# Kernel optimization log

Hardware: AMD Instinct MI355X
Metric: run time of the kernel (lower is better)

Reference implementation:

```python
import jax, jax.numpy as jnp
import numpy as np

B, S, M_DIM, N_DIM, K_NNZ = 8, 2048, 2048, 2048, 205


def setup_inputs() -> dict:
    key = jax.random.key(0)
    k1, k2, k3, k4 = jax.random.split(key, 4)
    x = jax.random.normal(k1, (B, S, M_DIM), dtype=jnp.float32)
    # CSR structure: K_NNZ unique, sorted column indices per row
    scores = jax.random.uniform(k2, (N_DIM, M_DIM))
    cols = jnp.sort(jnp.argsort(scores, axis=1)[:, :K_NNZ], axis=1)  # [N, K] unique per row
    indices = cols.reshape(-1).astype(jnp.int32)                      # [nnz]
    indptr = (jnp.arange(N_DIM + 1) * K_NNZ).astype(jnp.int32)        # [N+1]
    W_val = jax.random.normal(k3, (N_DIM * K_NNZ,), dtype=jnp.float32) * (1.0 / np.sqrt(M_DIM))
    bias = jax.random.normal(k4, (N_DIM,), dtype=jnp.float32) * 0.01
    return {"x": x, "W_val": W_val, "bias": bias, "indices": indices, "indptr": indptr}


def reference(x, W_val, bias, indices, indptr):
    # SparseLinear.forward: y = x @ W^T + bias, with W stored in CSR
    # (W_val: nnz values, indptr: [N+1] row pointers, indices: [nnz] column ids).
    N = indptr.shape[0] - 1
    M = x.shape[-1]
    nnz = W_val.shape[0]
    # row id of each nonzero, derived from indptr (standard CSR expansion)
    row_ids = jnp.searchsorted(indptr, jnp.arange(nnz, dtype=indptr.dtype), side="right") - 1
    # materialize the sparse weight (CSR columns are unique per row -> set is exact)
    W = jnp.zeros((N, M), dtype=W_val.dtype).at[row_ids, indices].set(W_val)
    return jnp.einsum("bsm,nm->bsn", x, W) + bias
```

## Files before the change

### kernel.cpp

```cpp
#include <hip/hip_runtime.h>
#include <hip/hip_bf16.h>
#include <stdint.h>

#define M_TOT 16384
#define K_TOT 2048
#define N_TOT 2048

#define BM 256
#define BN 256
#define BK 64
#define LDS_HALF (128 * 64)

typedef __attribute__((ext_vector_type(8))) short short8;
typedef __attribute__((ext_vector_type(4))) float float4v;
typedef __attribute__((ext_vector_type(8))) unsigned short ushort8;
typedef __attribute__((ext_vector_type(4))) unsigned short ushort4v;

__device__ __forceinline__ unsigned short f2bf_rne(float f) {
    union { float f; unsigned u; } a; a.f = f;
    unsigned r = a.u + 0x7FFFu + ((a.u >> 16) & 1u);
    return (unsigned short)(r >> 16);
}

__global__ __launch_bounds__(256) void densify_kernel(
    const float* __restrict__ val, const int* __restrict__ idx,
    const int* __restrict__ indptr, unsigned short* __restrict__ Wb) {
    const int n = blockIdx.x;
    unsigned short* row = Wb + (size_t)n * K_TOT;
    ushort8 z = {0, 0, 0, 0, 0, 0, 0, 0};
    ((ushort8*)row)[threadIdx.x] = z;
    __syncthreads();
    const int s = indptr[n], e = indptr[n + 1];
    for (int j = s + (int)threadIdx.x; j < e; j += (int)blockDim.x)
        row[idx[j]] = f2bf_rne(val[j]);
}

#define CAST_GRID 2048
__global__ __launch_bounds__(256) void cast_kernel(
    const float* __restrict__ x, unsigned short* __restrict__ xb) {
    const float4* xf = (const float4*)x;
    size_t i = (size_t)blockIdx.x * 256 + threadIdx.x;
    const size_t stride = (size_t)CAST_GRID * 256;
#pragma unroll
    for (int it = 0; it < 16; ++it, i += stride) {
        float4 a = xf[i];
        ushort4v o;
        o[0] = f2bf_rne(a.x); o[1] = f2bf_rne(a.y);
        o[2] = f2bf_rne(a.z); o[3] = f2bf_rne(a.w);
        ((ushort4v*)xb)[i] = o;
    }
}

__global__ __launch_bounds__(512, 2) void gemm_bias_kernel_256(
    const unsigned short* __restrict__ A,
    const unsigned short* __restrict__ Bw,
    const float* __restrict__ bias,
    float* __restrict__ C)
{
    extern __shared__ unsigned short lds[];

    const int tid  = threadIdx.x;
    const int lane = tid & 63;
    const int wave = tid >> 6;

    const int raw = blockIdx.x;
    const int lid = (raw & 7) * 64 + (raw >> 3);
    const int bm = lid >> 3;
    const int bn = lid & 7;

    const int wrow = wave >> 2;
    const int wcol = wave & 3;
    const int wr16 = wrow * 16;
    const int wc16 = wcol * 16;
    const int mrow = lane & 15;
    const int quad = lane >> 4;
    const int rx   = mrow & 7;

    const int srow = lane >> 3;
    const int csrc = ((lane & 7) ^ srow) * 8;
    const unsigned short* pA = A  + (size_t)(bm * BM + wave * 8 + srow) * K_TOT + csrc;
    const unsigned short* pB = Bw + (size_t)(bn * BN + wave * 8 + srow) * K_TOT + csrc;
    unsigned short* lw = lds + wave * 8 * 64;

    float4v acc[8][4] = {};
    short8 af[4][2];
    short8 bfr[2][2][2];

#define STAGE(PG, MATIDX, BUF, H, K0)                                            \
    { _Pragma("unroll")                                                          \
      for (int l = 0; l < 2; ++l) {                                              \
        const unsigned short* g = (PG) + ((size_t)((H) * 128 + l * 64) * K_TOT + (size_t)(K0)); \
        unsigned short* lp = lw + (((BUF) * 4 + (MATIDX) * 2 + (H)) * LDS_HALF) + l * 64 * 64;  \
        __builtin_amdgcn_global_load_lds(                                        \
            (const __attribute__((address_space(1))) unsigned int*)g,            \
            (__attribute__((address_space(3))) unsigned int*)lp, 16, 0, 0);      \
      } }

#define RD_A(RBUF, RMH)                                                          \
    { const unsigned short* Ah = lds + ((RBUF) * 4 + (RMH)) * LDS_HALF;          \
      _Pragma("unroll")                                                          \
      for (int mi = 0; mi < 4; ++mi) {                                           \
        const int r = mi * 32 + wr16 + mrow;                                     \
        _Pragma("unroll")                                                        \
        for (int ks = 0; ks < 2; ++ks)                                           \
          af[mi][ks] = *(const short8*)(Ah + r * 64 + (((ks * 4 + quad) ^ rx) * 8)); \
      } }

#define RD_B(RBUF, RNH)                                                          \
    { const unsigned short* Bh = lds + ((RBUF) * 4 + 2 + (RNH)) * LDS_HALF;      \
      _Pragma("unroll")                                                          \
      for (int ni = 0; ni < 2; ++ni) {                                           \
        const int r = ni * 64 + wc16 + mrow;                                     \
        _Pragma("unroll")                                                        \
        for (int ks = 0; ks < 2; ++ks)                                           \
          bfr[RNH][ni][ks] = *(const short8*)(Bh + r * 64 + (((ks * 4 + quad) ^ rx) * 8)); \
      } }

#define BARX { asm volatile("" ::: "memory"); __builtin_amdgcn_s_barrier(); asm volatile("" ::: "memory"); }
#define NOB  ((void)0);
#define WAITV4 asm volatile("s_waitcnt vmcnt(4)" ::: "memory")
#define WAITV0 asm volatile("s_waitcnt vmcnt(0)" ::: "memory")
#define WV4B { WAITV4; BARX }
#define WV0B { WAITV0; BARX }
#define NOWT ((void)0)
#define NOSTG ((void)0)
#define NORD ((void)0)

#define PHASE(MH, NH, BHEAD, STG, TAILW, RDS)                                    \
  {                                                                              \
    BHEAD                                                                        \
    asm volatile("s_waitcnt lgkmcnt(0)" ::: "memory");                           \
    __builtin_amdgcn_s_setprio(1);                                               \
    _Pragma("unroll")                                                            \
    for (int mi = 0; mi < 4; ++mi)                                               \
      _Pragma("unroll")                                                          \
      for (int ni = 0; ni < 2; ++ni)                                             \
        _Pragma("unroll")                                                        \
        for (int ks = 0; ks < 2; ++ks)                                           \
          acc[(MH) * 4 + mi][(NH) * 2 + ni] =                                    \
              __builtin_amdgcn_mfma_f32_16x16x32_bf16(                           \
                  af[mi][ks], bfr[NH][ni][ks], acc[(MH) * 4 + mi][(NH) * 2 + ni], 0, 0, 0); \
    __builtin_amdgcn_s_setprio(0);                                               \
    STG;                                                                         \
    TAILW;                                                                       \
    RDS;                                                                         \
  }

    STAGE(pA, 0, 0, 0, 0);
    STAGE(pB, 1, 0, 1, 0);
    STAGE(pB, 1, 0, 0, 0);
    STAGE(pA, 0, 0, 1, 0);
    STAGE(pA, 0, 1, 0, 64);
    STAGE(pB, 1, 1, 1, 64);
    WAITV4;
    BARX
    RD_A(0, 0); RD_B(0, 0);

    int k0b = 64, k0c = 128, k0d = 192;
#pragma unroll 1
    for (int it = 0; it < 15; ++it) {
        PHASE(0, 0, NOB,  STAGE(pB, 1, 1, 0, k0b), NOWT, RD_B(0, 1))
        PHASE(0, 1, BARX, STAGE(pA, 0, 1, 1, k0b), NOWT, RD_A(0, 1))
        PHASE(1, 1, BARX, STAGE(pA, 0, 0, 0, k0c), NOWT, NORD)
        PHASE(1, 0, BARX, STAGE(pB, 1, 0, 1, k0c), WV4B, RD_A(1, 0); RD_B(1, 0))
        PHASE(0, 0, NOB,  STAGE(pB, 1, 0, 0, k0c), NOWT, RD_B(1, 1))
        PHASE(0, 1, BARX, STAGE(pA, 0, 0, 1, k0c), NOWT, RD_A(1, 1))
        PHASE(1, 1, BARX, STAGE(pA, 0, 1, 0, k0d), NOWT, NORD)
        PHASE(1, 0, BARX, STAGE(pB, 1, 1, 1, k0d), WV4B, RD_A(0, 0); RD_B(0, 0))
        k0b += 128; k0c += 128; k0d += 128;
    }
    PHASE(0, 0, NOB,  STAGE(pB, 1, 1, 0, k0b), NOWT, RD_B(0, 1))
    PHASE(0, 1, BARX, STAGE(pA, 0, 1, 1, k0b), NOWT, RD_A(0, 1))
    PHASE(1, 1, BARX, NOSTG, NOWT, NORD)
    PHASE(1, 0, BARX, NOSTG, WV0B, RD_A(1, 0); RD_B(1, 0))
    PHASE(0, 0, NOB,  NOSTG, NOWT, RD_B(1, 1))
    PHASE(0, 1, BARX, NOSTG, NOWT, RD_A(1, 1))
    PHASE(1, 1, BARX, NOSTG, NOWT, NORD)
    PHASE(1, 0, BARX, NOSTG, NOWT, NORD)

#pragma unroll
    for (int nh = 0; nh < 2; ++nh)
#pragma unroll
        for (int ni = 0; ni < 2; ++ni) {
            const int col = bn * BN + nh * 128 + ni * 64 + wc16 + mrow;
            const float bv = bias[col];
#pragma unroll
            for (int mh = 0; mh < 2; ++mh)
#pragma unroll
                for (int mi = 0; mi < 4; ++mi) {
                    const int row0 = bm * BM + mh * 128 + mi * 32 + wr16 + quad * 4;
#pragma unroll
                    for (int r = 0; r < 4; ++r)
                        C[(size_t)(row0 + r) * N_TOT + col] =
                            acc[mh * 4 + mi][nh * 2 + ni][r] + bv;
                }
        }
#undef PHASE
#undef STAGE
#undef RD_A
#undef RD_B
#undef BARX
#undef NOB
#undef WAITV4
#undef WAITV0
#undef WV4B
#undef WV0B
#undef NOWT
#undef NOSTG
#undef NORD
}

#define FBM 128
#define FBN 128
#define FBK 64
__global__ __launch_bounds__(256) void gemm_bias_kernel_128(
    const unsigned short* __restrict__ A,
    const unsigned short* __restrict__ Bw,
    const float* __restrict__ bias,
    float* __restrict__ C)
{
    __shared__ unsigned short Asm[FBM * FBK];
    __shared__ unsigned short Bsm[FBN * FBK];

    const int tid  = threadIdx.x;
    const int lane = tid & 63;
    const int wave = tid >> 6;
    const int bm = blockIdx.y;
    const int bn = blockIdx.x;

    const int srow_l = lane >> 3;
    const int schunk = ((lane & 7) ^ srow_l) * 8;
    const unsigned short* a_g[4];
    const unsigned short* b_g[4];
    unsigned short* a_l[4];
    unsigned short* b_l[4];
#pragma unroll
    for (int l = 0; l < 4; ++l) {
        const int row = wave * 32 + l * 8 + srow_l;
        a_g[l] = A  + (size_t)(bm * FBM + row) * K_TOT + schunk;
        b_g[l] = Bw + (size_t)(bn * FBN + row) * K_TOT + schunk;
        a_l[l] = Asm + (wave * 32 + l * 8) * FBK;
        b_l[l] = Bsm + (wave * 32 + l * 8) * FBK;
    }

    const int wm = (wave >> 1) * 64;
    const int wn = (wave & 1) * 64;
    const int mrow = lane & 15;
    const int quad = lane >> 4;
    const int rx   = mrow & 7;

    float4v acc[4][4] = {};

    for (int k0 = 0; k0 < K_TOT; k0 += FBK) {
        __syncthreads();
#pragma unroll
        for (int l = 0; l < 4; ++l)
            __builtin_amdgcn_global_load_lds(
                (const __attribute__((address_space(1))) unsigned int*)(a_g[l] + k0),
                (__attribute__((address_space(3))) unsigned int*)a_l[l], 16, 0, 0);
#pragma unroll
        for (int l = 0; l < 4; ++l)
            __builtin_amdgcn_global_load_lds(
                (const __attribute__((address_space(1))) unsigned int*)(b_g[l] + k0),
                (__attribute__((address_space(3))) unsigned int*)b_l[l], 16, 0, 0);
        __syncthreads();

#pragma unroll
        for (int ks = 0; ks < 2; ++ks) {
            short8 af[4], bf_[4];
#pragma unroll
            for (int mi = 0; mi < 4; ++mi) {
                const int r = wm + mi * 16 + mrow;
                const int slot = (ks * 4 + quad) ^ rx;
                af[mi] = *(const short8*)(Asm + r * FBK + slot * 8);
            }
#pragma unroll
            for (int ni = 0; ni < 4; ++ni) {
                const int r = wn + ni * 16 + mrow;
                const int slot = (ks * 4 + quad) ^ rx;
                bf_[ni] = *(const short8*)(Bsm + r * FBK + slot * 8);
            }
#pragma unroll
            for (int mi = 0; mi < 4; ++mi)
#pragma unroll
                for (int ni = 0; ni < 4; ++ni)
                    acc[mi][ni] = __builtin_amdgcn_mfma_f32_16x16x32_bf16(
                        af[mi], bf_[ni], acc[mi][ni], 0, 0, 0);
        }
    }

#pragma unroll
    for (int ni = 0; ni < 4; ++ni) {
        const int col = bn * FBN + wn + ni * 16 + mrow;
        const float bv = bias[col];
#pragma unroll
        for (int mi = 0; mi < 4; ++mi) {
#pragma unroll
            for (int r = 0; r < 4; ++r) {
                const int row = bm * FBM + wm + mi * 16 + quad * 4 + r;
                C[(size_t)row * N_TOT + col] = acc[mi][ni][r] + bv;
            }
        }
    }
}

extern "C" void kernel_launch(void* const* d_in, const int* in_sizes, int n_in,
                              void* d_out, int out_size, void* d_ws, size_t ws_size,
                              hipStream_t stream) {
    const float* x       = (const float*)d_in[0];
    const float* W_val   = (const float*)d_in[1];
    const float* bias    = (const float*)d_in[2];
    const int*   indices = (const int*)d_in[3];
    const int*   indptr  = (const int*)d_in[4];
    float* out = (float*)d_out;

    unsigned short* xb = (unsigned short*)d_ws;
    unsigned short* Wb = xb + (size_t)M_TOT * K_TOT;
    if (ws_size < ((size_t)M_TOT * K_TOT + (size_t)N_TOT * K_TOT) * sizeof(unsigned short))
        return;

    hipError_t attr_ok = hipFuncSetAttribute(
        reinterpret_cast<const void*>(gemm_bias_kernel_256),
        hipFuncAttributeMaxDynamicSharedMemorySize, 131072);

    cast_kernel<<<CAST_GRID, 256, 0, stream>>>(x, xb);
    densify_kernel<<<N_TOT, 256, 0, stream>>>(W_val, indices, indptr, Wb);

    if (attr_ok == hipSuccess) {
        gemm_bias_kernel_256<<<dim3(512), 512, 131072, stream>>>(xb, Wb, bias, out);
    } else {
        dim3 grid(N_TOT / FBN, M_TOT / FBM);
        gemm_bias_kernel_128<<<grid, 256, 0, stream>>>(xb, Wb, bias, out);
    }
}
```

Measured before the change: 346.8 us.

## Merge cast and densify kernels and interleave LDS fragment reads with MFMAs

The separate x-cast and CSR-densify kernels become one prep kernel. Its first block range builds the bf16 weight rows and the rest casts x eight elements per thread, which removes one launch and lets the two jobs overlap. In the GEMM main loop, the LDS reads of the next B and A fragments now sit between MFMA groups inside a phase instead of after all MFMAs, to hide LDS latency under matrix work. The risk is register pressure or new dependency stalls, because af slots are overwritten while later MFMAs in the same phase still issue.

```diff
diff --git a/kernel.cpp b/kernel.cpp
--- a/kernel.cpp
+++ b/kernel.cpp
@@ -11,10 +11,12 @@
 #define BK 64
 #define LDS_HALF (128 * 64)
 
+#define W_BLOCKS 2048
+#define CAST_BLOCKS 16384
+
 typedef __attribute__((ext_vector_type(8))) short short8;
 typedef __attribute__((ext_vector_type(4))) float float4v;
 typedef __attribute__((ext_vector_type(8))) unsigned short ushort8;
-typedef __attribute__((ext_vector_type(4))) unsigned short ushort4v;
 
 __device__ __forceinline__ unsigned short f2bf_rne(float f) {
     union { float f; unsigned u; } a; a.f = f;
@@ -22,32 +24,30 @@
     return (unsigned short)(r >> 16);
 }
 
-__global__ __launch_bounds__(256) void densify_kernel(
+__global__ __launch_bounds__(256) void prep_kernel(
+    const float* __restrict__ x,
     const float* __restrict__ val, const int* __restrict__ idx,
-    const int* __restrict__ indptr, unsigned short* __restrict__ Wb) {
-    const int n = blockIdx.x;
-    unsigned short* row = Wb + (size_t)n * K_TOT;
-    ushort8 z = {0, 0, 0, 0, 0, 0, 0, 0};
-    ((ushort8*)row)[threadIdx.x] = z;
-    __syncthreads();
-    const int s = indptr[n], e = indptr[n + 1];
-    for (int j = s + (int)threadIdx.x; j < e; j += (int)blockDim.x)
-        row[idx[j]] = f2bf_rne(val[j]);
-}
-
-#define CAST_GRID 2048
-__global__ __launch_bounds__(256) void cast_kernel(
-    const float* __restrict__ x, unsigned short* __restrict__ xb) {
-    const float4* xf = (const float4*)x;
-    size_t i = (size_t)blockIdx.x * 256 + threadIdx.x;
-    const size_t stride = (size_t)CAST_GRID * 256;
-#pragma unroll
-    for (int it = 0; it < 16; ++it, i += stride) {
-        float4 a = xf[i];
-        ushort4v o;
-        o[0] = f2bf_rne(a.x); o[1] = f2bf_rne(a.y);
-        o[2] = f2bf_rne(a.z); o[3] = f2bf_rne(a.w);
-        ((ushort4v*)xb)[i] = o;
+    const int* __restrict__ indptr,
+    unsigned short* __restrict__ xb, unsigned short* __restrict__ Wb) {
+    const int b = blockIdx.x;
+    if (b < W_BLOCKS) {
+        const int n = b;
+        unsigned short* row = Wb + (size_t)n * K_TOT;
+        ushort8 z = {0, 0, 0, 0, 0, 0, 0, 0};
+        ((ushort8*)row)[threadIdx.x] = z;
+        __syncthreads();
+        const int s = indptr[n], e = indptr[n + 1];
+        for (int j = s + (int)threadIdx.x; j < e; j += (int)blockDim.x)
+            row[idx[j]] = f2bf_rne(val[j]);
+    } else {
+        const int i = (b - W_BLOCKS) * 256 + (int)threadIdx.x;
+        const float4* xf = (const float4*)x;
+        float4 a = xf[2 * i];
+        float4 c = xf[2 * i + 1];
+        ushort8 o;
+        o[0] = f2bf_rne(a.x); o[1] = f2bf_rne(a.y); o[2] = f2bf_rne(a.z); o[3] = f2bf_rne(a.w);
+        o[4] = f2bf_rne(c.x); o[5] = f2bf_rne(c.y); o[6] = f2bf_rne(c.z); o[7] = f2bf_rne(c.w);
+        ((ushort8*)xb)[i] = o;
     }
 }
 
@@ -106,6 +106,13 @@
           af[mi][ks] = *(const short8*)(Ah + r * 64 + (((ks * 4 + quad) ^ rx) * 8)); \
       } }
 
+#define RD_A1(RBUF, RMH, MI)                                                     \
+    { const unsigned short* Ah = lds + ((RBUF) * 4 + (RMH)) * LDS_HALF;          \
+      const int r = (MI) * 32 + wr16 + mrow;                                     \
+      _Pragma("unroll")                                                          \
+      for (int ks = 0; ks < 2; ++ks)                                             \
+        af[MI][ks] = *(const short8*)(Ah + r * 64 + (((ks * 4 + quad) ^ rx) * 8)); }
+
 #define RD_B(RBUF, RNH)                                                          \
     { const unsigned short* Bh = lds + ((RBUF) * 4 + 2 + (RNH)) * LDS_HALF;      \
       _Pragma("unroll")                                                          \
@@ -116,6 +123,15 @@
           bfr[RNH][ni][ks] = *(const short8*)(Bh + r * 64 + (((ks * 4 + quad) ^ rx) * 8)); \
       } }
 
+#define MFMA_MI(MH, NH, MI)                                                      \
+    _Pragma("unroll")                                                            \
+    for (int ni = 0; ni < 2; ++ni)                                               \
+      _Pragma("unroll")                                                          \
+      for (int ks = 0; ks < 2; ++ks)                                             \
+        acc[(MH) * 4 + (MI)][(NH) * 2 + ni] =                                    \
+            __builtin_amdgcn_mfma_f32_16x16x32_bf16(                             \
+                af[MI][ks], bfr[NH][ni][ks], acc[(MH) * 4 + (MI)][(NH) * 2 + ni], 0, 0, 0);
+
 #define BARX { asm volatile("" ::: "memory"); __builtin_amdgcn_s_barrier(); asm volatile("" ::: "memory"); }
 #define NOB  ((void)0);
 #define WAITV4 asm volatile("s_waitcnt vmcnt(4)" ::: "memory")
@@ -126,25 +142,36 @@
 #define NOSTG ((void)0)
 #define NORD ((void)0)
 
-#define PHASE(MH, NH, BHEAD, STG, TAILW, RDS)                                    \
-  {                                                                              \
+#define PH_HEAD(BHEAD)                                                           \
     BHEAD                                                                        \
     asm volatile("s_waitcnt lgkmcnt(0)" ::: "memory");                           \
-    __builtin_amdgcn_s_setprio(1);                                               \
-    _Pragma("unroll")                                                            \
-    for (int mi = 0; mi < 4; ++mi)                                               \
-      _Pragma("unroll")                                                          \
-      for (int ni = 0; ni < 2; ++ni)                                             \
-        _Pragma("unroll")                                                        \
-        for (int ks = 0; ks < 2; ++ks)                                           \
-          acc[(MH) * 4 + mi][(NH) * 2 + ni] =                                    \
-              __builtin_amdgcn_mfma_f32_16x16x32_bf16(                           \
-                  af[mi][ks], bfr[NH][ni][ks], acc[(MH) * 4 + mi][(NH) * 2 + ni], 0, 0, 0); \
+    __builtin_amdgcn_s_setprio(1);
+
+#define PH_TAIL(STG, TAILW, TAILRD)                                              \
     __builtin_amdgcn_s_setprio(0);                                               \
     STG;                                                                         \
     TAILW;                                                                       \
-    RDS;                                                                         \
-  }
+    TAILRD;
+
+#define PHASE_NR(MH, NH, BHEAD, STG, TAILW, TAILRD)                              \
+  { PH_HEAD(BHEAD)                                                               \
+    MFMA_MI(MH, NH, 0) MFMA_MI(MH, NH, 1) MFMA_MI(MH, NH, 2) MFMA_MI(MH, NH, 3) \
+    PH_TAIL(STG, TAILW, TAILRD) }
+
+#define PHASE_RB(MH, NH, BHEAD, RBUF, RNH, STG, TAILW)                           \
+  { PH_HEAD(BHEAD)                                                               \
+    MFMA_MI(MH, NH, 0)                                                           \
+    RD_B(RBUF, RNH)                                                              \
+    MFMA_MI(MH, NH, 1) MFMA_MI(MH, NH, 2) MFMA_MI(MH, NH, 3)                     \
+    PH_TAIL(STG, NOWT, NORD) }
+
+#define PHASE_RA(MH, NH, BHEAD, RBUF, RMH, STG, TAILW)                           \
+  { PH_HEAD(BHEAD)                                                               \
+    MFMA_MI(MH, NH, 0) RD_A1(RBUF, RMH, 0)                                       \
+    MFMA_MI(MH, NH, 1) RD_A1(RBUF, RMH, 1)                                       \
+    MFMA_MI(MH, NH, 2) RD_A1(RBUF, RMH, 2)                                       \
+    MFMA_MI(MH, NH, 3) RD_A1(RBUF, RMH, 3)                                       \
+    PH_TAIL(STG, NOWT, NORD) }
 
     STAGE(pA, 0, 0, 0, 0);
     STAGE(pB, 1, 0, 1, 0);
@@ -159,24 +186,24 @@
     int k0b = 64, k0c = 128, k0d = 192;
 #pragma unroll 1
     for (int it = 0; it < 15; ++it) {
-        PHASE(0, 0, NOB,  STAGE(pB, 1, 1, 0, k0b), NOWT, RD_B(0, 1))
-        PHASE(0, 1, BARX, STAGE(pA, 0, 1, 1, k0b), NOWT, RD_A(0, 1))
-        PHASE(1, 1, BARX, STAGE(pA, 0, 0, 0, k0c), NOWT, NORD)
-        PHASE(1, 0, BARX, STAGE(pB, 1, 0, 1, k0c), WV4B, RD_A(1, 0); RD_B(1, 0))
-        PHASE(0, 0, NOB,  STAGE(pB, 1, 0, 0, k0c), NOWT, RD_B(1, 1))
-        PHASE(0, 1, BARX, STAGE(pA, 0, 0, 1, k0c), NOWT, RD_A(1, 1))
-        PHASE(1, 1, BARX, STAGE(pA, 0, 1, 0, k0d), NOWT, NORD)
-        PHASE(1, 0, BARX, STAGE(pB, 1, 1, 1, k0d), WV4B, RD_A(0, 0); RD_B(0, 0))
+        PHASE_RB(0, 0, NOB,  0, 1, STAGE(pB, 1, 1, 0, k0b), NOWT)
+        PHASE_RA(0, 1, BARX, 0, 1, STAGE(pA, 0, 1, 1, k0b), NOWT)
+        PHASE_NR(1, 1, BARX, STAGE(pA, 0, 0, 0, k0c), NOWT, NORD)
+        PHASE_NR(1, 0, BARX, STAGE(pB, 1, 0, 1, k0c), WV4B, RD_A(1, 0); RD_B(1, 0))
+        PHASE_RB(0, 0, NOB,  1, 1, STAGE(pB, 1, 0, 0, k0c), NOWT)
+        PHASE_RA(0, 1, BARX, 1, 1, STAGE(pA, 0, 0, 1, k0c), NOWT)
+        PHASE_NR(1, 1, BARX, STAGE(pA, 0, 1, 0, k0d), NOWT, NORD)
+        PHASE_NR(1, 0, BARX, STAGE(pB, 1, 1, 1, k0d), WV4B, RD_A(0, 0); RD_B(0, 0))
         k0b += 128; k0c += 128; k0d += 128;
     }
-    PHASE(0, 0, NOB,  STAGE(pB, 1, 1, 0, k0b), NOWT, RD_B(0, 1))
-    PHASE(0, 1, BARX, STAGE(pA, 0, 1, 1, k0b), NOWT, RD_A(0, 1))
-    PHASE(1, 1, BARX, NOSTG, NOWT, NORD)
-    PHASE(1, 0, BARX, NOSTG, WV0B, RD_A(1, 0); RD_B(1, 0))
-    PHASE(0, 0, NOB,  NOSTG, NOWT, RD_B(1, 1))
-    PHASE(0, 1, BARX, NOSTG, NOWT, RD_A(1, 1))
-    PHASE(1, 1, BARX, NOSTG, NOWT, NORD)
-    PHASE(1, 0, BARX, NOSTG, NOWT, NORD)
+    PHASE_RB(0, 0, NOB,  0, 1, STAGE(pB, 1, 1, 0, k0b), NOWT)
+    PHASE_RA(0, 1, BARX, 0, 1, STAGE(pA, 0, 1, 1, k0b), NOWT)
+    PHASE_NR(1, 1, BARX, NOSTG, NOWT, NORD)
+    PHASE_NR(1, 0, BARX, NOSTG, WV0B, RD_A(1, 0); RD_B(1, 0))
+    PHASE_RB(0, 0, NOB,  1, 1, NOSTG, NOWT)
+    PHASE_RA(0, 1, BARX, 1, 1, NOSTG, NOWT)
+    PHASE_NR(1, 1, BARX, NOSTG, NOWT, NORD)
+    PHASE_NR(1, 0, BARX, NOSTG, NOWT, NORD)
 
 #pragma unroll
     for (int nh = 0; nh < 2; ++nh)
@@ -195,9 +222,15 @@
                             acc[mh * 4 + mi][nh * 2 + ni][r] + bv;
                 }
         }
-#undef PHASE
+#undef PHASE_NR
+#undef PHASE_RB
+#undef PHASE_RA
+#undef PH_HEAD
+#undef PH_TAIL
+#undef MFMA_MI
 #undef STAGE
 #undef RD_A
+#undef RD_A1
 #undef RD_B
 #undef BARX
 #undef NOB
@@ -323,8 +356,7 @@
         reinterpret_cast<const void*>(gemm_bias_kernel_256),
         hipFuncAttributeMaxDynamicSharedMemorySize, 131072);
 
-    cast_kernel<<<CAST_GRID, 256, 0, stream>>>(x, xb);
-    densify_kernel<<<N_TOT, 256, 0, stream>>>(W_val, indices, indptr, Wb);
+    prep_kernel<<<W_BLOCKS + CAST_BLOCKS, 256, 0, stream>>>(x, W_val, indices, indptr, xb, Wb);
 
     if (attr_ok == hipSuccess) {
         gemm_bias_kernel_256<<<dim3(512), 512, 131072, stream>>>(xb, Wb, bias, out);
```

After: 337.6 us. 1.03x faster.
